# Kernel tuning notes

Measured on AMD Instinct MI355X. Metric: run time of the kernel, lower is better.

Reference implementation:

```python
import jax, jax.numpy as jnp
import numpy as np

B, LA, LB, DIM, INNER, OUTER = 64, 1024, 1024, 640, 256, 1024
NEG = -1e30


def setup_inputs() -> dict:
    key = jax.random.key(0)
    ks = jax.random.split(key, 10)
    s = 1.0 / np.sqrt(DIM)
    return {
        "a_pad": jax.random.normal(ks[0], (B, LA, DIM), jnp.float32),
        "b_pad": jax.random.normal(ks[1], (B, LB, DIM), jnp.float32),
        "len_a": jax.random.randint(ks[2], (B,), 1, LA + 1, jnp.int32),
        "len_b": jax.random.randint(ks[3], (B,), 1, LB + 1, jnp.int32),
        "Wq": jax.random.normal(ks[4], (DIM, INNER), jnp.float32) * s,
        "bq": jax.random.normal(ks[5], (INNER,), jnp.float32) * 0.01,
        "Wk": jax.random.normal(ks[6], (DIM, INNER), jnp.float32) * s,
        "bk": jax.random.normal(ks[7], (INNER,), jnp.float32) * 0.01,
        "Wv": jax.random.normal(ks[8], (DIM, OUTER), jnp.float32) * s,
        "bv": jax.random.normal(ks[9], (OUTER,), jnp.float32) * 0.01,
    }


def reference(a_pad, b_pad, len_a, len_b, Wq, bq, Wk, bk, Wv, bv):
    inner_dim = Wq.shape[1]
    scale = 1.0 / jnp.sqrt(jnp.asarray(inner_dim, a_pad.dtype))

    qa = a_pad @ Wq + bq   # [B, LA, INNER]
    ka = a_pad @ Wk + bk
    va = a_pad @ Wv + bv   # [B, LA, OUTER]
    qb = b_pad @ Wq + bq   # [B, LB, INNER]
    kb = b_pad @ Wk + bk
    vb = b_pad @ Wv + bv

    La, Lb = a_pad.shape[1], b_pad.shape[1]
    valid_a = jnp.arange(La)[None, :] < len_a[:, None]  # [B, LA]
    valid_b = jnp.arange(Lb)[None, :] < len_b[:, None]  # [B, LB]

    # a attends over b: softmax over valid b keys, mean over valid a queries
    sc_a = jnp.einsum('bqd,bkd->bqk', qa * scale, kb)          # [B, LA, LB]
    sc_a = jnp.where(valid_b[:, None, :], sc_a, NEG)
    attn_a = jax.nn.softmax(sc_a, axis=-1)
    cross_a = jnp.einsum('bqk,bkv->bqv', attn_a, vb)            # [B, LA, OUTER]
    emb_a = jnp.einsum('bq,bqv->bv', valid_a.astype(cross_a.dtype), cross_a)
    emb_a = emb_a / len_a[:, None].astype(emb_a.dtype)          # [B, OUTER]

    # b attends over a
    sc_b = jnp.einsum('bqd,bkd->bqk', qb * scale, ka)           # [B, LB, LA]
    sc_b = jnp.where(valid_a[:, None, :], sc_b, NEG)
    attn_b = jax.nn.softmax(sc_b, axis=-1)
    cross_b = jnp.einsum('bqk,bkv->bqv', attn_b, va)            # [B, LB, OUTER]
    emb_b = jnp.einsum('bq,bqv->bv', valid_b.astype(cross_b.dtype), cross_b)
    emb_b = emb_b / len_b[:, None].astype(emb_b.dtype)

    return (emb_a, emb_b)
```

## Files before the change

### kernel.cpp

```cpp
#include <hip/hip_runtime.h>
#include <hip/hip_bf16.h>
#include <math.h>

#define BATCH 64
#define L 1024
#define DIM 640
#define INNER 256
#define OUTER 1024
#define QKW 512

typedef __attribute__((ext_vector_type(8))) short bf16x8;
typedef __attribute__((ext_vector_type(4))) float f32x4;

__device__ __forceinline__ float bf2f(unsigned short u) {
    union { unsigned int i; float f; } v; v.i = ((unsigned int)u) << 16; return v.f;
}
__device__ __forceinline__ unsigned short f2bf(float f) {
    __hip_bfloat16 h = __float2bfloat16(f);
    return *reinterpret_cast<unsigned short*>(&h);
}
__device__ __forceinline__ void gload_lds16(const void* g, void* l) {
    __builtin_amdgcn_global_load_lds(
        (const __attribute__((address_space(1))) void*)g,
        (__attribute__((address_space(3))) void*)l, 16, 0, 0);
}

__global__ __launch_bounds__(256)
void cvt_bf16_kernel(const float* __restrict__ src, unsigned short* __restrict__ dst,
                     const int* __restrict__ len)
{
    const int bx = blockIdx.x, b = blockIdx.y;
    const int R = (len[b] + 127) & ~127;
    if (bx * 8 >= R * 5) return;
    const size_t i = (size_t)b * (L * DIM / 4) + bx * 256 + threadIdx.x;
    float4 v = ((const float4*)src)[i];
    ushort4 o;
    o.x = f2bf(v.x); o.y = f2bf(v.y); o.z = f2bf(v.z); o.w = f2bf(v.w);
    ((ushort4*)dst)[i] = o;
}

__global__ __launch_bounds__(256)
void wt_kernel(const float* __restrict__ Wq, const float* __restrict__ Wk,
               unsigned short* __restrict__ Wt)
{
    int idx = blockIdx.x * 256 + threadIdx.x;
    if (idx >= QKW * DIM) return;
    int n = idx / DIM, k = idx - n * DIM;
    float v = (n < INNER) ? Wq[(size_t)k * INNER + n]
                          : Wk[(size_t)k * INNER + (n - INNER)];
    Wt[idx] = f2bf(v);
}

__global__ __launch_bounds__(256)
void projqk_kernel(const unsigned short* __restrict__ X,
                   const unsigned short* __restrict__ Wt,
                   const float* __restrict__ bq, const float* __restrict__ bk,
                   const int* __restrict__ len,
                   unsigned short* __restrict__ Y)
{
    __shared__ unsigned short As[128 * 32];
    __shared__ unsigned short Bs[128 * 32];
    const int bid = blockIdx.x;
    const int xcd = bid & 7, idx = bid >> 3;
    const int widx = xcd * 256 + idx;
    const int nt = widx & 3, mt = widx >> 2;
    const int batch = mt >> 3, mloc = mt & 7;
    if (mloc * 128 >= len[batch]) return;

    const int tid = threadIdx.x;
    const int w = tid >> 6, l = tid & 63;
    const int bm = mt * 128, bn = nt * 128;
    const int wr = w >> 1, wc = w & 1;

    const unsigned short* Ag = X  + (size_t)(bm + w*16 + (l>>2)) * DIM + (l&3)*8;
    const unsigned short* Bg = Wt + (size_t)(bn + w*16 + (l>>2)) * DIM + (l&3)*8;
    unsigned short* Al0 = As + w*512;
    unsigned short* Al1 = As + 2048 + w*512;
    unsigned short* Bl0 = Bs + w*512;
    unsigned short* Bl1 = Bs + 2048 + w*512;

    f32x4 acc[4][4] = {};

    for (int k0 = 0; k0 < DIM; k0 += 32) {
        gload_lds16(Ag + k0,                  Al0);
        gload_lds16(Ag + (size_t)64*DIM + k0, Al1);
        gload_lds16(Bg + k0,                  Bl0);
        gload_lds16(Bg + (size_t)64*DIM + k0, Bl1);
        __syncthreads();
        bf16x8 af[4], bfr[4];
        #pragma unroll
        for (int m = 0; m < 4; ++m)
            af[m] = *(const bf16x8*)&As[(wr*64 + m*16 + (l&15))*32 + (l>>4)*8];
        #pragma unroll
        for (int n = 0; n < 4; ++n)
            bfr[n] = *(const bf16x8*)&Bs[(wc*64 + n*16 + (l&15))*32 + (l>>4)*8];
        #pragma unroll
        for (int m = 0; m < 4; ++m)
            #pragma unroll
            for (int n = 0; n < 4; ++n)
                acc[m][n] = __builtin_amdgcn_mfma_f32_16x16x32_bf16(af[m], bfr[n], acc[m][n], 0, 0, 0);
        __syncthreads();
    }

    #pragma unroll
    for (int m = 0; m < 4; ++m)
        #pragma unroll
        for (int n = 0; n < 4; ++n) {
            const int col = bn + wc*64 + n*16 + (l&15);
            const float bias = (col < INNER) ? bq[col] : bk[col - INNER];
            #pragma unroll
            for (int j = 0; j < 4; ++j) {
                const int row = bm + wr*64 + m*16 + (l>>4)*4 + j;
                Y[(size_t)row * QKW + col] = f2bf(acc[m][n][j] + bias);
            }
        }
}

__global__ __launch_bounds__(256)
void scores_kernel(const unsigned short* __restrict__ QKq,
                   const unsigned short* __restrict__ QKk,
                   const int* __restrict__ len_q,
                   const int* __restrict__ len_k,
                   unsigned short* __restrict__ E,
                   float* __restrict__ lsum, int b0)
{
    __shared__ unsigned short As[128 * 32];
    __shared__ unsigned short Bs[128 * 32];
    const int bz = blockIdx.z, b = b0 + bz;
    const int bm = blockIdx.x * 128, bn = blockIdx.y * 128;
    const int lq = len_q[b], lenk = len_k[b];
    if (bm >= lq || bn >= lenk) return;

    const int tid = threadIdx.x;
    const int w = tid >> 6, l = tid & 63;
    const int wr = w >> 1, wc = w & 1;

    const unsigned short* Qg = QKq + ((size_t)b * L + bm + w*16 + (l>>2)) * QKW + (l&3)*8;
    const unsigned short* Kg = QKk + ((size_t)b * L + bn + w*16 + (l>>2)) * QKW + INNER + (l&3)*8;
    unsigned short* Al0 = As + w*512;
    unsigned short* Al1 = As + 2048 + w*512;
    unsigned short* Bl0 = Bs + w*512;
    unsigned short* Bl1 = Bs + 2048 + w*512;

    f32x4 acc[4][4] = {};

    for (int k0 = 0; k0 < INNER; k0 += 32) {
        gload_lds16(Qg + k0,                  Al0);
        gload_lds16(Qg + (size_t)64*QKW + k0, Al1);
        gload_lds16(Kg + k0,                  Bl0);
        gload_lds16(Kg + (size_t)64*QKW + k0, Bl1);
        __syncthreads();
        bf16x8 af[4], bfr[4];
        #pragma unroll
        for (int m = 0; m < 4; ++m)
            af[m] = *(const bf16x8*)&As[(wr*64 + m*16 + (l&15))*32 + (l>>4)*8];
        #pragma unroll
        for (int n = 0; n < 4; ++n)
            bfr[n] = *(const bf16x8*)&Bs[(wc*64 + n*16 + (l&15))*32 + (l>>4)*8];
        #pragma unroll
        for (int m = 0; m < 4; ++m)
            #pragma unroll
            for (int n = 0; n < 4; ++n)
                acc[m][n] = __builtin_amdgcn_mfma_f32_16x16x32_bf16(af[m], bfr[n], acc[m][n], 0, 0, 0);
        __syncthreads();
    }

    const float scale = 0.0625f;
    float rs[4][4];
    #pragma unroll
    for (int m = 0; m < 4; ++m)
        #pragma unroll
        for (int j = 0; j < 4; ++j) rs[m][j] = 0.f;

    #pragma unroll
    for (int m = 0; m < 4; ++m)
        #pragma unroll
        for (int n = 0; n < 4; ++n) {
            const int col = bn + wc*64 + n*16 + (l&15);
            const bool valid = col < lenk;
            #pragma unroll
            for (int j = 0; j < 4; ++j) {
                const float e = valid ? __expf(acc[m][n][j] * scale) : 0.f;
                rs[m][j] += e;
                const int row = bm + wr*64 + m*16 + (l>>4)*4 + j;
                E[((size_t)bz * L + row) * L + col] = f2bf(e);
            }
        }

    #pragma unroll
    for (int m = 0; m < 4; ++m)
        #pragma unroll
        for (int j = 0; j < 4; ++j) {
            float v = rs[m][j];
            v += __shfl_xor(v, 1); v += __shfl_xor(v, 2);
            v += __shfl_xor(v, 4); v += __shfl_xor(v, 8);
            if ((l & 15) == 0) {
                const int row = bm + wr*64 + m*16 + (l>>4)*4 + j;
                atomicAdd(&lsum[(size_t)b * L + row], v);
            }
        }
}

__global__ __launch_bounds__(256)
void colsum_kernel(const unsigned short* __restrict__ E, const float* __restrict__ lsum,
                   const int* __restrict__ len_q, const int* __restrict__ len_k,
                   float* __restrict__ w, int b0)
{
    const int bz = blockIdx.y, b = b0 + bz;
    const int qc = blockIdx.x * 128;
    const int lq = len_q[b];
    if (qc >= lq) return;
    const int k4 = threadIdx.x * 4;
    if (k4 >= len_k[b]) return;
    const int qe = (qc + 128 < lq) ? qc + 128 : lq;
    const unsigned short* Eb = E + (size_t)bz * L * L + k4;
    const float* lb = lsum + (size_t)b * L;
    const float inv_lq = 1.0f / (float)lq;
    float a0 = 0.f, a1 = 0.f, a2 = 0.f, a3 = 0.f;
    for (int q = qc; q < qe; ++q) {
        ushort4 ev = *(const ushort4*)(Eb + (size_t)q * L);
        float r = inv_lq / lb[q];
        a0 += bf2f(ev.x) * r; a1 += bf2f(ev.y) * r;
        a2 += bf2f(ev.z) * r; a3 += bf2f(ev.w) * r;
    }
    float* wb = w + (size_t)b * L + k4;
    atomicAdd(wb + 0, a0); atomicAdd(wb + 1, a1);
    atomicAdd(wb + 2, a2); atomicAdd(wb + 3, a3);
}

__global__ __launch_bounds__(256)
void pool_kernel(const float* __restrict__ w, const float* __restrict__ X,
                 float* __restrict__ pooled)
{
    const int b   = blockIdx.y;
    const int kc  = blockIdx.x * 128;
    const int tid = threadIdx.x;
    const float* wb = w + (size_t)b * L + kc;
    const float* Xb = X + ((size_t)b * L + kc) * DIM;
    float acc0 = 0.f, acc1 = 0.f, acc2 = 0.f;
    for (int kk = 0; kk < 128; ++kk) {
        float wgt = wb[kk];
        if (wgt == 0.f) continue;
        const float* row = Xb + (size_t)kk * DIM;
        acc0 += wgt * row[tid];
        acc1 += wgt * row[tid + 256];
        if (tid < 128) acc2 += wgt * row[tid + 512];
    }
    atomicAdd(&pooled[(size_t)b * DIM + tid],       acc0);
    atomicAdd(&pooled[(size_t)b * DIM + tid + 256], acc1);
    if (tid < 128) atomicAdd(&pooled[(size_t)b * DIM + tid + 512], acc2);
}

__global__ __launch_bounds__(256)
void outproj_kernel(const float* __restrict__ pooled, const float* __restrict__ Wv,
                    const float* __restrict__ bv, float* __restrict__ out)
{
    const int r = blockIdx.x;
    const int o = blockIdx.y * 256 + threadIdx.x;
    const float* p = pooled + (size_t)r * DIM;
    float a0 = bv[o], a1 = 0.f, a2 = 0.f, a3 = 0.f;
    for (int d = 0; d < DIM; d += 4) {
        a0 = fmaf(p[d+0], Wv[(size_t)(d+0)*OUTER + o], a0);
        a1 = fmaf(p[d+1], Wv[(size_t)(d+1)*OUTER + o], a1);
        a2 = fmaf(p[d+2], Wv[(size_t)(d+2)*OUTER + o], a2);
        a3 = fmaf(p[d+3], Wv[(size_t)(d+3)*OUTER + o], a3);
    }
    out[(size_t)r * OUTER + o] = (a0+a1)+(a2+a3);
}

extern "C" void kernel_launch(void* const* d_in, const int* in_sizes, int n_in,
                              void* d_out, int out_size, void* d_ws, size_t ws_size,
                              hipStream_t stream)
{
    (void)in_sizes; (void)n_in; (void)out_size;
    const float* a_pad = (const float*)d_in[0];
    const float* b_pad = (const float*)d_in[1];
    const int*   len_a = (const int*)d_in[2];
    const int*   len_b = (const int*)d_in[3];
    const float* Wq    = (const float*)d_in[4];
    const float* bq    = (const float*)d_in[5];
    const float* Wk    = (const float*)d_in[6];
    const float* bk    = (const float*)d_in[7];
    const float* Wv    = (const float*)d_in[8];
    const float* bv    = (const float*)d_in[9];
    float* out = (float*)d_out;

    char* ws = (char*)d_ws;
    size_t off = 0;
    auto alloc = [&](size_t bytes) -> void* {
        void* p = (void*)(ws + off);
        off += (bytes + 255) & ~(size_t)255;
        return p;
    };

    const size_t XE = (size_t)BATCH * L * DIM;
    const size_t QE = (size_t)BATCH * L * QKW;
    unsigned short* Xa  = (unsigned short*)alloc(XE * 2);
    unsigned short* Xb  = (unsigned short*)alloc(XE * 2);
    unsigned short* Wt  = (unsigned short*)alloc((size_t)QKW * DIM * 2);
    unsigned short* QKa = (unsigned short*)alloc(QE * 2);
    unsigned short* QKb = (unsigned short*)alloc(QE * 2);
    float* l2     = (float*)alloc((size_t)2 * BATCH * L * 4);
    float* w2     = (float*)alloc((size_t)2 * BATCH * L * 4);
    float* pooled = (float*)alloc((size_t)2 * BATCH * DIM * 4);
    unsigned short* E = (unsigned short*)(ws + off);
    size_t eAvail = (ws_size > off) ? (ws_size - off) : 0;
    int gb = (int)(eAvail / ((size_t)L * L * 2));
    if (gb < 1) gb = 1;
    if (gb > BATCH) gb = BATCH;

    cvt_bf16_kernel<<<dim3(640, BATCH), 256, 0, stream>>>(a_pad, Xa, len_a);
    cvt_bf16_kernel<<<dim3(640, BATCH), 256, 0, stream>>>(b_pad, Xb, len_b);
    wt_kernel<<<(QKW * DIM + 255) / 256, 256, 0, stream>>>(Wq, Wk, Wt);

    projqk_kernel<<<2048, 256, 0, stream>>>(Xa, Wt, bq, bk, len_a, QKa);
    projqk_kernel<<<2048, 256, 0, stream>>>(Xb, Wt, bq, bk, len_b, QKb);

    hipMemsetAsync(l2,     0, (size_t)2 * BATCH * L * 4,   stream);
    hipMemsetAsync(w2,     0, (size_t)2 * BATCH * L * 4,   stream);
    hipMemsetAsync(pooled, 0, (size_t)2 * BATCH * DIM * 4, stream);

    for (int dir = 0; dir < 2; ++dir) {
        const unsigned short* QKq = (dir == 0) ? QKa : QKb;
        const unsigned short* QKk = (dir == 0) ? QKb : QKa;
        const int* lenq = (dir == 0) ? len_a : len_b;
        const int* lenk = (dir == 0) ? len_b : len_a;
        float* lsum = l2 + (size_t)dir * BATCH * L;
        float* wv   = w2 + (size_t)dir * BATCH * L;
        for (int b0 = 0; b0 < BATCH; b0 += gb) {
            int g = (gb < BATCH - b0) ? gb : (BATCH - b0);
            scores_kernel<<<dim3(8, 8, g), 256, 0, stream>>>(QKq, QKk, lenq, lenk, E, lsum, b0);
            colsum_kernel<<<dim3(8, g), 256, 0, stream>>>(E, lsum, lenq, lenk, wv, b0);
        }
    }

    pool_kernel<<<dim3(8, BATCH), 256, 0, stream>>>(w2,                   b_pad, pooled);
    pool_kernel<<<dim3(8, BATCH), 256, 0, stream>>>(w2 + (size_t)BATCH*L, a_pad, pooled + (size_t)BATCH*DIM);
    outproj_kernel<<<dim3(128, 4), 256, 0, stream>>>(pooled, Wv, bv, out);
}
```

Before: 787.3 us.

## Fuse fp32-to-bf16 conversion into projection GEMM and double-buffer swizzled LDS tiles

```diff
diff --git a/kernel.cpp b/kernel.cpp
--- a/kernel.cpp
+++ b/kernel.cpp
@@ -1,6 +1,5 @@
 #include <hip/hip_runtime.h>
 #include <hip/hip_bf16.h>
-#include <math.h>
 
 #define BATCH 64
 #define L 1024
@@ -26,20 +25,6 @@
 }
 
 __global__ __launch_bounds__(256)
-void cvt_bf16_kernel(const float* __restrict__ src, unsigned short* __restrict__ dst,
-                     const int* __restrict__ len)
-{
-    const int bx = blockIdx.x, b = blockIdx.y;
-    const int R = (len[b] + 127) & ~127;
-    if (bx * 8 >= R * 5) return;
-    const size_t i = (size_t)b * (L * DIM / 4) + bx * 256 + threadIdx.x;
-    float4 v = ((const float4*)src)[i];
-    ushort4 o;
-    o.x = f2bf(v.x); o.y = f2bf(v.y); o.z = f2bf(v.z); o.w = f2bf(v.w);
-    ((ushort4*)dst)[i] = o;
-}
-
-__global__ __launch_bounds__(256)
 void wt_kernel(const float* __restrict__ Wq, const float* __restrict__ Wk,
                unsigned short* __restrict__ Wt)
 {
@@ -52,14 +37,14 @@
 }
 
 __global__ __launch_bounds__(256)
-void projqk_kernel(const unsigned short* __restrict__ X,
+void projqk_kernel(const float* __restrict__ X,
                    const unsigned short* __restrict__ Wt,
                    const float* __restrict__ bq, const float* __restrict__ bk,
                    const int* __restrict__ len,
                    unsigned short* __restrict__ Y)
 {
-    __shared__ unsigned short As[128 * 32];
-    __shared__ unsigned short Bs[128 * 32];
+    __shared__ unsigned short As[2][8192];
+    __shared__ unsigned short Bs[2][8192];
     const int bid = blockIdx.x;
     const int xcd = bid & 7, idx = bid >> 3;
     const int widx = xcd * 256 + idx;
@@ -71,35 +56,70 @@
     const int w = tid >> 6, l = tid & 63;
     const int bm = mt * 128, bn = nt * 128;
     const int wr = w >> 1, wc = w & 1;
-
-    const unsigned short* Ag = X  + (size_t)(bm + w*16 + (l>>2)) * DIM + (l&3)*8;
-    const unsigned short* Bg = Wt + (size_t)(bn + w*16 + (l>>2)) * DIM + (l&3)*8;
-    unsigned short* Al0 = As + w*512;
-    unsigned short* Al1 = As + 2048 + w*512;
-    unsigned short* Bl0 = Bs + w*512;
-    unsigned short* Bl1 = Bs + 2048 + w*512;
+    const int swz = ((l & 7) ^ ((l >> 3) & 7)) * 8;
+
+    const unsigned short* Bg = Wt + (size_t)(bn + w*8 + (l>>3)) * DIM + swz;
+    const int ar = tid >> 1, ah = tid & 1;
+    const float* Ax = X + (size_t)(bm + ar) * DIM + ah * 32;
+
+    auto STAGE_B = [&](int buf, int k0) {
+        #pragma unroll
+        for (int i = 0; i < 4; ++i)
+            gload_lds16(Bg + (size_t)(i*32) * DIM + k0, &Bs[buf][w*512 + i*2048]);
+    };
+    auto LOAD_A = [&](float4* d, int k0) {
+        #pragma unroll
+        for (int j = 0; j < 8; ++j) d[j] = *(const float4*)(Ax + k0 + j*4);
+    };
+    auto WRITE_A = [&](int buf, const float4* s) {
+        #pragma unroll
+        for (int j = 0; j < 4; ++j) {
+            union { bf16x8 v; unsigned short u[8]; } pk;
+            float4 x = s[2*j], y = s[2*j+1];
+            pk.u[0]=f2bf(x.x); pk.u[1]=f2bf(x.y); pk.u[2]=f2bf(x.z); pk.u[3]=f2bf(x.w);
+            pk.u[4]=f2bf(y.x); pk.u[5]=f2bf(y.y); pk.u[6]=f2bf(y.z); pk.u[7]=f2bf(y.w);
+            *(bf16x8*)&As[buf][ar*64 + (((ah*4 + j) ^ (ar & 7)) * 8)] = pk.v;
+        }
+    };
 
     f32x4 acc[4][4] = {};
-
-    for (int k0 = 0; k0 < DIM; k0 += 32) {
-        gload_lds16(Ag + k0,                  Al0);
-        gload_lds16(Ag + (size_t)64*DIM + k0, Al1);
-        gload_lds16(Bg + k0,                  Bl0);
-        gload_lds16(Bg + (size_t)64*DIM + k0, Bl1);
+    auto COMPUTE = [&](int buf) {
+        #pragma unroll
+        for (int kk2 = 0; kk2 < 2; ++kk2) {
+            const int slot = ((kk2*4 + (l>>4)) ^ (l & 7)) * 8;
+            bf16x8 af[4], bfr[4];
+            #pragma unroll
+            for (int m = 0; m < 4; ++m)
+                af[m] = *(const bf16x8*)&As[buf][(wr*64 + m*16 + (l&15))*64 + slot];
+            #pragma unroll
+            for (int n = 0; n < 4; ++n)
+                bfr[n] = *(const bf16x8*)&Bs[buf][(wc*64 + n*16 + (l&15))*64 + slot];
+            #pragma unroll
+            for (int m = 0; m < 4; ++m)
+                #pragma unroll
+                for (int n = 0; n < 4; ++n)
+                    acc[m][n] = __builtin_amdgcn_mfma_f32_16x16x32_bf16(af[m], bfr[n], acc[m][n], 0, 0, 0);
+        }
+    };
+
+    float4 va0[8], va1[8];
+    LOAD_A(va0, 0);
+    STAGE_B(0, 0);
+    WRITE_A(0, va0);
+    __syncthreads();
+
+    #pragma unroll
+    for (int t = 0; t < 10; t += 2) {
+        if (t + 1 < 10) { LOAD_A(va1, (t+1)*64); STAGE_B(1, (t+1)*64); }
+        COMPUTE(0);
+        if (t + 1 < 10) WRITE_A(1, va1);
         __syncthreads();
-        bf16x8 af[4], bfr[4];
-        #pragma unroll
-        for (int m = 0; m < 4; ++m)
-            af[m] = *(const bf16x8*)&As[(wr*64 + m*16 + (l&15))*32 + (l>>4)*8];
-        #pragma unroll
-        for (int n = 0; n < 4; ++n)
-            bfr[n] = *(const bf16x8*)&Bs[(wc*64 + n*16 + (l&15))*32 + (l>>4)*8];
-        #pragma unroll
-        for (int m = 0; m < 4; ++m)
-            #pragma unroll
-            for (int n = 0; n < 4; ++n)
-                acc[m][n] = __builtin_amdgcn_mfma_f32_16x16x32_bf16(af[m], bfr[n], acc[m][n], 0, 0, 0);
-        __syncthreads();
+        if (t + 1 < 10) {
+            if (t + 2 < 10) { LOAD_A(va0, (t+2)*64); STAGE_B(0, (t+2)*64); }
+            COMPUTE(1);
+            if (t + 2 < 10) WRITE_A(0, va0);
+            __syncthreads();
+        }
     }
 
     #pragma unroll
@@ -124,8 +144,8 @@
                    unsigned short* __restrict__ E,
                    float* __restrict__ lsum, int b0)
 {
-    __shared__ unsigned short As[128 * 32];
-    __shared__ unsigned short Bs[128 * 32];
+    __shared__ unsigned short As[2][8192];
+    __shared__ unsigned short Bs[2][8192];
     const int bz = blockIdx.z, b = b0 + bz;
     const int bm = blockIdx.x * 128, bn = blockIdx.y * 128;
     const int lq = len_q[b], lenk = len_k[b];
@@ -134,34 +154,45 @@
     const int tid = threadIdx.x;
     const int w = tid >> 6, l = tid & 63;
     const int wr = w >> 1, wc = w & 1;
-
-    const unsigned short* Qg = QKq + ((size_t)b * L + bm + w*16 + (l>>2)) * QKW + (l&3)*8;
-    const unsigned short* Kg = QKk + ((size_t)b * L + bn + w*16 + (l>>2)) * QKW + INNER + (l&3)*8;
-    unsigned short* Al0 = As + w*512;
-    unsigned short* Al1 = As + 2048 + w*512;
-    unsigned short* Bl0 = Bs + w*512;
-    unsigned short* Bl1 = Bs + 2048 + w*512;
+    const int swz = ((l & 7) ^ ((l >> 3) & 7)) * 8;
+
+    const unsigned short* Qg = QKq + ((size_t)b * L + bm + w*8 + (l>>3)) * QKW + swz;
+    const unsigned short* Kg = QKk + ((size_t)b * L + bn + w*8 + (l>>3)) * QKW + INNER + swz;
+
+    auto STAGE = [&](int buf, int k0) {
+        #pragma unroll
+        for (int i = 0; i < 4; ++i) {
+            gload_lds16(Qg + (size_t)(i*32) * QKW + k0, &As[buf][w*512 + i*2048]);
+            gload_lds16(Kg + (size_t)(i*32) * QKW + k0, &Bs[buf][w*512 + i*2048]);
+        }
+    };
 
     f32x4 acc[4][4] = {};
-
-    for (int k0 = 0; k0 < INNER; k0 += 32) {
-        gload_lds16(Qg + k0,                  Al0);
-        gload_lds16(Qg + (size_t)64*QKW + k0, Al1);
-        gload_lds16(Kg + k0,                  Bl0);
-        gload_lds16(Kg + (size_t)64*QKW + k0, Bl1);
-        __syncthreads();
-        bf16x8 af[4], bfr[4];
-        #pragma unroll
-        for (int m = 0; m < 4; ++m)
-            af[m] = *(const bf16x8*)&As[(wr*64 + m*16 + (l&15))*32 + (l>>4)*8];
-        #pragma unroll
-        for (int n = 0; n < 4; ++n)
-            bfr[n] = *(const bf16x8*)&Bs[(wc*64 + n*16 + (l&15))*32 + (l>>4)*8];
-        #pragma unroll
-        for (int m = 0; m < 4; ++m)
+    auto COMPUTE = [&](int buf) {
+        #pragma unroll
+        for (int kk2 = 0; kk2 < 2; ++kk2) {
+            const int slot = ((kk2*4 + (l>>4)) ^ (l & 7)) * 8;
+            bf16x8 af[4], bfr[4];
+            #pragma unroll
+            for (int m = 0; m < 4; ++m)
+                af[m] = *(const bf16x8*)&As[buf][(wr*64 + m*16 + (l&15))*64 + slot];
             #pragma unroll
             for (int n = 0; n < 4; ++n)
-                acc[m][n] = __builtin_amdgcn_mfma_f32_16x16x32_bf16(af[m], bfr[n], acc[m][n], 0, 0, 0);
+                bfr[n] = *(const bf16x8*)&Bs[buf][(wc*64 + n*16 + (l&15))*64 + slot];
+            #pragma unroll
+            for (int m = 0; m < 4; ++m)
+                #pragma unroll
+                for (int n = 0; n < 4; ++n)
+                    acc[m][n] = __builtin_amdgcn_mfma_f32_16x16x32_bf16(af[m], bfr[n], acc[m][n], 0, 0, 0);
+        }
+    };
+
+    STAGE(0, 0);
+    __syncthreads();
+    #pragma unroll
+    for (int t = 0; t < 4; ++t) {
+        if (t < 3) STAGE((t+1) & 1, (t+1)*64);
+        COMPUTE(t & 1);
         __syncthreads();
     }
 
@@ -293,10 +324,7 @@
         return p;
     };
 
-    const size_t XE = (size_t)BATCH * L * DIM;
     const size_t QE = (size_t)BATCH * L * QKW;
-    unsigned short* Xa  = (unsigned short*)alloc(XE * 2);
-    unsigned short* Xb  = (unsigned short*)alloc(XE * 2);
     unsigned short* Wt  = (unsigned short*)alloc((size_t)QKW * DIM * 2);
     unsigned short* QKa = (unsigned short*)alloc(QE * 2);
     unsigned short* QKb = (unsigned short*)alloc(QE * 2);
@@ -309,12 +337,10 @@
     if (gb < 1) gb = 1;
     if (gb > BATCH) gb = BATCH;
 
-    cvt_bf16_kernel<<<dim3(640, BATCH), 256, 0, stream>>>(a_pad, Xa, len_a);
-    cvt_bf16_kernel<<<dim3(640, BATCH), 256, 0, stream>>>(b_pad, Xb, len_b);
     wt_kernel<<<(QKW * DIM + 255) / 256, 256, 0, stream>>>(Wq, Wk, Wt);
 
-    projqk_kernel<<<2048, 256, 0, stream>>>(Xa, Wt, bq, bk, len_a, QKa);
-    projqk_kernel<<<2048, 256, 0, stream>>>(Xb, Wt, bq, bk, len_b, QKb);
+    projqk_kernel<<<2048, 256, 0, stream>>>(a_pad, Wt, bq, bk, len_a, QKa);
+    projqk_kernel<<<2048, 256, 0, stream>>>(b_pad, Wt, bq, bk, len_b, QKb);
 
     hipMemsetAsync(l2,     0, (size_t)2 * BATCH * L * 4,   stream);
     hipMemsetAsync(w2,     0, (size_t)2 * BATCH * L * 4,   stream);
```

Result: slower. 855.0 us (+8.6%).
